# Kernel optimization log

Hardware: AMD Instinct MI355X
Metric: run time of the kernel (lower is better)

## Reference

```python
import jax, jax.numpy as jnp
import numpy as np

NUM_GRAPHS = 64
NODES_PER_GRAPH = 512


def _all_pair_edges(num_graphs, n):
    """Flat src/dst indices for all directed pairs (i,j), i!=j, per graph,
    in the same row-major order as generate_edgelist in the torch code."""
    i = np.repeat(np.arange(n), n)
    j = np.tile(np.arange(n), n)
    keep = i != j
    si, sj = i[keep], j[keep]                      # [n*(n-1)]
    off = (np.arange(num_graphs) * n)[:, None]     # per-graph node offset
    src = (off + si[None, :]).reshape(-1)
    dst = (off + sj[None, :]).reshape(-1)
    return src.astype(np.int32), dst.astype(np.int32)


def setup_inputs() -> dict:
    key = jax.random.key(0)
    k1, k2 = jax.random.split(key)
    n_nodes = NUM_GRAPHS * NODES_PER_GRAPH
    p = jax.random.normal(k1, (n_nodes, 2), dtype=jnp.float32)
    src_np, dst_np = _all_pair_edges(NUM_GRAPHS, NODES_PER_GRAPH)
    n_edges = src_np.shape[0]
    # edge_attr[:,0] = ideal length l > 0, edge_attr[:,1] = stiffness k > 0
    edge_attr = jax.random.uniform(k2, (n_edges, 2), dtype=jnp.float32,
                                   minval=0.5, maxval=2.0)
    return {
        "p": p,
        "edge_attr": edge_attr,
        "src": jnp.asarray(src_np),
        "dst": jnp.asarray(dst_np),
    }


def reference(p, edge_attr, src, dst):
    # gather all-pair node coords (node2edge)
    start = p[src]                                  # [E,2]
    end = p[dst]                                    # [E,2]
    term1 = (start[:, 0] - end[:, 0]) ** 2
    term2 = (start[:, 1] - end[:, 1]) ** 2
    l = edge_attr[:, 0]
    k = edge_attr[:, 1]
    term3 = l ** 2
    term4 = 2.0 * l * jnp.sqrt(term1 + term2)
    energy = k / 2.0 * (term1 + term2 + term3 - term4)
    return energy.sum()
```

## Files before the change

### kernel.cpp

```cpp
#include <hip/hip_runtime.h>


#define NPG   512
#define EPR   (NPG - 1)
#define EPG   (NPG * EPR)
#define BPG   32
#define ROWS  (NPG / BPG)
#define CHUNK_EDGES (ROWS * EPR)
#define CHUNK_Q     (CHUNK_EDGES / 2)

#define LDS_PAD(x) ((x) + ((x) >> 4))

__device__ __forceinline__ float edge_pair(float4 v, int le0, int row0,
                                           const float2* __restrict__ lds_p)
{
    float e;
    {
        const int m = (le0 * 8209) >> 22;
        const int r = le0 - ((m << 9) - m);
        const int i = row0 + m;
        const int j = r + (r >= i);
        float2 ps = lds_p[LDS_PAD(i)];
        float2 pd = lds_p[LDS_PAD(j)];
        float dx = ps.x - pd.x, dy = ps.y - pd.y;
        float s = __builtin_amdgcn_sqrtf(dx * dx + dy * dy);
        float d = s - v.x;
        e = (0.5f * v.y) * d * d;
    }
    {
        const int le1 = le0 + 1;
        const int m = (le1 * 8209) >> 22;
        const int r = le1 - ((m << 9) - m);
        const int i = row0 + m;
        const int j = r + (r >= i);
        float2 ps = lds_p[LDS_PAD(i)];
        float2 pd = lds_p[LDS_PAD(j)];
        float dx = ps.x - pd.x, dy = ps.y - pd.y;
        float s = __builtin_amdgcn_sqrtf(dx * dx + dy * dy);
        float d = s - v.z;
        e += (0.5f * v.w) * d * d;
    }
    return e;
}

__global__ __launch_bounds__(256) void energy_main(
    const float2* __restrict__ p2,
    const float2* __restrict__ ea2,
    float* __restrict__ partial)
{
    const int bx  = blockIdx.x;
    const int g   = bx >> 5;
    const int blk = bx & (BPG - 1);
    const int t   = threadIdx.x;
    const int row0 = blk * ROWS;

    __shared__ float2 lds_p[LDS_PAD(NPG - 1) + 10];

    {
        const float2* srcp = p2 + (size_t)g * NPG;
        lds_p[LDS_PAD(t)]       = srcp[t];
        lds_p[LDS_PAD(t + 256)] = srcp[t + 256];
    }
    __syncthreads();

    const float4* ea4 = (const float4*)ea2 +
                        ((size_t)g * (EPG / 2) + (size_t)blk * CHUNK_Q);

    float acc = 0.0f;

#pragma unroll
    for (int s = 0; s < 4; ++s) {
        const int q0 = t + s * 1024;
        const int q1 = q0 + 256;
        const int q2 = q0 + 512;
        const int q3 = q0 + 768;
        const bool ok3 = (q3 < CHUNK_Q);
        const int q3c = ok3 ? q3 : (CHUNK_Q - 1);

        float4 v0 = ea4[q0];
        float4 v1 = ea4[q1];
        float4 v2 = ea4[q2];
        float4 v3 = ea4[q3c];

        acc += edge_pair(v0, 2 * q0, row0, lds_p);
        acc += edge_pair(v1, 2 * q1, row0, lds_p);
        acc += edge_pair(v2, 2 * q2, row0, lds_p);
        float e3 = edge_pair(v3, 2 * q3c, row0, lds_p);
        acc += ok3 ? e3 : 0.0f;
    }

    for (int off = 32; off > 0; off >>= 1)
        acc += __shfl_down(acc, off, 64);

    __shared__ float wsum[4];
    if ((t & 63) == 0) wsum[t >> 6] = acc;
    __syncthreads();

    if (t == 0)
        partial[bx] = wsum[0] + wsum[1] + wsum[2] + wsum[3];
}

__global__ __launch_bounds__(256) void energy_finish(
    const float4* __restrict__ partial4,
    float* __restrict__ out,
    int n)
{
    const int t = threadIdx.x;
    float acc = 0.0f;
    for (int i = t * 4; i < n; i += 1024) {
        float4 v = partial4[i >> 2];
        acc += (v.x + v.y) + (v.z + v.w);
    }
    for (int off = 32; off > 0; off >>= 1)
        acc += __shfl_down(acc, off, 64);

    __shared__ float wsum[4];
    if ((t & 63) == 0) wsum[t >> 6] = acc;
    __syncthreads();

    if (t == 0)
        out[0] = wsum[0] + wsum[1] + wsum[2] + wsum[3];
}

extern "C" void kernel_launch(void* const* d_in, const int* in_sizes, int n_in,
                              void* d_out, int out_size, void* d_ws, size_t ws_size,
                              hipStream_t stream) {
    const float2* p2  = (const float2*)d_in[0];
    const float2* ea2 = (const float2*)d_in[1];
    float* out     = (float*)d_out;
    float* partial = (float*)d_ws;

    const int n_nodes    = in_sizes[0] / 2;
    const int num_graphs = n_nodes / NPG;
    const int grid       = num_graphs * BPG;

    energy_main<<<grid, 256, 0, stream>>>(p2, ea2, partial);
    energy_finish<<<1, 256, 0, stream>>>((const float4*)partial, out, grid);
}
```

Before: 27.75 us.

## Fuse reduction into a cooperative grid-synced kernel with fewer, larger blocks

Cuts the grid from 2048 to 512 blocks, so each block now processes four row-chunks of one graph and reuses its LDS node load across them. The two-kernel launch becomes a single cooperative kernel that uses a grid-wide sync before block 0 does the final reduction, with the old two-kernel path kept as a fallback. The second edge's index math in each pair is also derived from the first instead of recomputed. The aim is to remove one launch and cut repeated LDS staging, but grid sync and the per-call host attribute and occupancy queries add overhead, and fewer blocks may expose less memory-level parallelism.

```diff
diff --git a/kernel.cpp b/kernel.cpp
--- a/kernel.cpp
+++ b/kernel.cpp
@@ -1,25 +1,28 @@
 #include <hip/hip_runtime.h>
+#include <hip/hip_cooperative_groups.h>
+
+namespace cg = cooperative_groups;
 
 
 #define NPG   512
 #define EPR   (NPG - 1)
 #define EPG   (NPG * EPR)
-#define BPG   32
-#define ROWS  (NPG / BPG)
+#define ROWS  16
 #define CHUNK_EDGES (ROWS * EPR)
 #define CHUNK_Q     (CHUNK_EDGES / 2)
+#define NBLK  512
 
 #define LDS_PAD(x) ((x) + ((x) >> 4))
 
 __device__ __forceinline__ float edge_pair(float4 v, int le0, int row0,
                                            const float2* __restrict__ lds_p)
 {
+    const int m0 = (le0 * 8209) >> 22;
+    const int r0 = le0 - ((m0 << 9) - m0);
     float e;
     {
-        const int m = (le0 * 8209) >> 22;
-        const int r = le0 - ((m << 9) - m);
-        const int i = row0 + m;
-        const int j = r + (r >= i);
+        const int i = row0 + m0;
+        const int j = r0 + (r0 >= i);
         float2 ps = lds_p[LDS_PAD(i)];
         float2 pd = lds_p[LDS_PAD(j)];
         float dx = ps.x - pd.x, dy = ps.y - pd.y;
@@ -28,10 +31,9 @@
         e = (0.5f * v.y) * d * d;
     }
     {
-        const int le1 = le0 + 1;
-        const int m = (le1 * 8209) >> 22;
-        const int r = le1 - ((m << 9) - m);
-        const int i = row0 + m;
+        const bool wrap = (r0 == EPR - 1);
+        const int i = row0 + m0 + (wrap ? 1 : 0);
+        const int r = wrap ? 0 : (r0 + 1);
         const int j = r + (r >= i);
         float2 ps = lds_p[LDS_PAD(i)];
         float2 pd = lds_p[LDS_PAD(j)];
@@ -43,19 +45,15 @@
     return e;
 }
 
-__global__ __launch_bounds__(256) void energy_main(
+__device__ __forceinline__ float block_energy(
     const float2* __restrict__ p2,
     const float2* __restrict__ ea2,
-    float* __restrict__ partial)
+    int b, int t)
 {
-    const int bx  = blockIdx.x;
-    const int g   = bx >> 5;
-    const int blk = bx & (BPG - 1);
-    const int t   = threadIdx.x;
-    const int row0 = blk * ROWS;
+    const int g = b >> 3;
+    const int chunk0 = (b & 7) * 4;
 
     __shared__ float2 lds_p[LDS_PAD(NPG - 1) + 10];
-
     {
         const float2* srcp = p2 + (size_t)g * NPG;
         lds_p[LDS_PAD(t)]       = srcp[t];
@@ -63,30 +61,35 @@
     }
     __syncthreads();
 
-    const float4* ea4 = (const float4*)ea2 +
-                        ((size_t)g * (EPG / 2) + (size_t)blk * CHUNK_Q);
+    const float4* gbase = (const float4*)ea2 + (size_t)g * (EPG / 2);
 
     float acc = 0.0f;
 
 #pragma unroll
-    for (int s = 0; s < 4; ++s) {
-        const int q0 = t + s * 1024;
-        const int q1 = q0 + 256;
-        const int q2 = q0 + 512;
-        const int q3 = q0 + 768;
-        const bool ok3 = (q3 < CHUNK_Q);
-        const int q3c = ok3 ? q3 : (CHUNK_Q - 1);
+    for (int ch = 0; ch < 4; ++ch) {
+        const int row0 = (chunk0 + ch) * ROWS;
+        const float4* ea4 = gbase + (size_t)(chunk0 + ch) * CHUNK_Q;
 
-        float4 v0 = ea4[q0];
-        float4 v1 = ea4[q1];
-        float4 v2 = ea4[q2];
-        float4 v3 = ea4[q3c];
+#pragma unroll
+        for (int s = 0; s < 4; ++s) {
+            const int q0 = t + s * 1024;
+            const int q1 = q0 + 256;
+            const int q2 = q0 + 512;
+            const int q3 = q0 + 768;
+            const bool ok3 = (q3 < CHUNK_Q);
+            const int q3c = ok3 ? q3 : (CHUNK_Q - 1);
 
-        acc += edge_pair(v0, 2 * q0, row0, lds_p);
-        acc += edge_pair(v1, 2 * q1, row0, lds_p);
-        acc += edge_pair(v2, 2 * q2, row0, lds_p);
-        float e3 = edge_pair(v3, 2 * q3c, row0, lds_p);
-        acc += ok3 ? e3 : 0.0f;
+            float4 v0 = ea4[q0];
+            float4 v1 = ea4[q1];
+            float4 v2 = ea4[q2];
+            float4 v3 = ea4[q3c];
+
+            acc += edge_pair(v0, 2 * q0, row0, lds_p);
+            acc += edge_pair(v1, 2 * q1, row0, lds_p);
+            acc += edge_pair(v2, 2 * q2, row0, lds_p);
+            float e3 = edge_pair(v3, 2 * q3c, row0, lds_p);
+            acc += ok3 ? e3 : 0.0f;
+        }
     }
 
     for (int off = 32; off > 0; off >>= 1)
@@ -96,30 +99,73 @@
     if ((t & 63) == 0) wsum[t >> 6] = acc;
     __syncthreads();
 
+    return wsum[0] + wsum[1] + wsum[2] + wsum[3];
+}
+
+__global__ __launch_bounds__(256, 2) void energy_coop(
+    const float2* __restrict__ p2,
+    const float2* __restrict__ ea2,
+    float* __restrict__ partial,
+    float* __restrict__ out)
+{
+    const int b = blockIdx.x;
+    const int t = threadIdx.x;
+
+    float bsum = block_energy(p2, ea2, b, t);
     if (t == 0)
-        partial[bx] = wsum[0] + wsum[1] + wsum[2] + wsum[3];
+        __hip_atomic_store(&partial[b], bsum, __ATOMIC_RELEASE,
+                           __HIP_MEMORY_SCOPE_AGENT);
+
+    cg::this_grid().sync();
+
+    if (b == 0) {
+        float a = 0.0f;
+        if (t < NBLK / 4) {
+#pragma unroll
+            for (int u = 0; u < 4; ++u)
+                a += __hip_atomic_load(&partial[t * 4 + u], __ATOMIC_RELAXED,
+                                       __HIP_MEMORY_SCOPE_AGENT);
+        }
+        for (int off = 32; off > 0; off >>= 1)
+            a += __shfl_down(a, off, 64);
+
+        __shared__ float fsum[4];
+        if ((t & 63) == 0) fsum[t >> 6] = a;
+        __syncthreads();
+        if (t == 0)
+            out[0] = fsum[0] + fsum[1] + fsum[2] + fsum[3];
+    }
+}
+
+
+__global__ __launch_bounds__(256, 2) void energy_main(
+    const float2* __restrict__ p2,
+    const float2* __restrict__ ea2,
+    float* __restrict__ partial)
+{
+    float bsum = block_energy(p2, ea2, blockIdx.x, threadIdx.x);
+    if (threadIdx.x == 0)
+        partial[blockIdx.x] = bsum;
 }
 
 __global__ __launch_bounds__(256) void energy_finish(
     const float4* __restrict__ partial4,
-    float* __restrict__ out,
-    int n)
+    float* __restrict__ out)
 {
     const int t = threadIdx.x;
-    float acc = 0.0f;
-    for (int i = t * 4; i < n; i += 1024) {
-        float4 v = partial4[i >> 2];
-        acc += (v.x + v.y) + (v.z + v.w);
+    float a = 0.0f;
+    if (t < NBLK / 4) {
+        float4 v = partial4[t];
+        a = (v.x + v.y) + (v.z + v.w);
     }
     for (int off = 32; off > 0; off >>= 1)
-        acc += __shfl_down(acc, off, 64);
+        a += __shfl_down(a, off, 64);
 
-    __shared__ float wsum[4];
-    if ((t & 63) == 0) wsum[t >> 6] = acc;
+    __shared__ float fsum[4];
+    if ((t & 63) == 0) fsum[t >> 6] = a;
     __syncthreads();
-
     if (t == 0)
-        out[0] = wsum[0] + wsum[1] + wsum[2] + wsum[3];
+        out[0] = fsum[0] + fsum[1] + fsum[2] + fsum[3];
 }
 
 extern "C" void kernel_launch(void* const* d_in, const int* in_sizes, int n_in,
@@ -130,10 +176,23 @@
     float* out     = (float*)d_out;
     float* partial = (float*)d_ws;
 
-    const int n_nodes    = in_sizes[0] / 2;
-    const int num_graphs = n_nodes / NPG;
-    const int grid       = num_graphs * BPG;
+    int dev = 0;
+    hipGetDevice(&dev);
+    int coopAttr = 0;
+    hipDeviceGetAttribute(&coopAttr, hipDeviceAttributeCooperativeLaunch, dev);
+    int numCU = 0;
+    hipDeviceGetAttribute(&numCU, hipDeviceAttributeMultiprocessorCount, dev);
+    int maxBlk = 0;
+    hipOccupancyMaxActiveBlocksPerMultiprocessor(&maxBlk, energy_coop, 256, 0);
 
-    energy_main<<<grid, 256, 0, stream>>>(p2, ea2, partial);
-    energy_finish<<<1, 256, 0, stream>>>((const float4*)partial, out, grid);
+    if (coopAttr && (long)maxBlk * numCU >= NBLK) {
+        void* args[] = { (void*)&p2, (void*)&ea2, (void*)&partial, (void*)&out };
+        hipError_t err = hipLaunchCooperativeKernel((const void*)energy_coop,
+                                                    dim3(NBLK), dim3(256),
+                                                    args, 0, stream);
+        if (err == hipSuccess) return;
+    }
+
+    energy_main<<<NBLK, 256, 0, stream>>>(p2, ea2, partial);
+    energy_finish<<<1, 256, 0, stream>>>((const float4*)partial, out);
 }
```

Result: faster. 26.93 us (-3.0%).
